# Kernel tuning notes

Measured on AMD Instinct MI355X. Metric: run time of the kernel, lower is better.

## Reference

```python
import jax, jax.numpy as jnp
import numpy as np

# Tree: 64 leaves (16 feat -> 16 out), 8 mids (16 feat + 8*16 child = 144 -> 32 out),
# root (16 feat + 8*32 child = 272 -> 64 out), head -> 10 tasks. Eval-mode BatchNorm.
B = 16384
EPS = 1e-5


def setup_inputs() -> dict:
    key = jax.random.key(0)
    ks = jax.random.split(key, 24)
    rn = lambda k, s: jax.random.normal(k, s, dtype=jnp.float32)
    ru = lambda k, s: jax.random.uniform(k, s, dtype=jnp.float32)
    return {
        "x": rn(ks[0], (B, 1168)),
        # leaf layers (64 nodes, 16 -> 16)
        "Wl": rn(ks[1], (64, 16, 16)) * 0.1, "bl": rn(ks[2], (64, 16)) * 0.1,
        "gl": ru(ks[3], (64, 16)) + 0.5, "betal": rn(ks[4], (64, 16)) * 0.1,
        "ml": rn(ks[5], (64, 16)) * 0.1, "vl": ru(ks[6], (64, 16)) + 0.5,
        # mid layers (8 nodes, 144 -> 32)
        "Wm": rn(ks[7], (8, 144, 32)) * 0.1, "bm": rn(ks[8], (8, 32)) * 0.1,
        "gm": ru(ks[9], (8, 32)) + 0.5, "betam": rn(ks[10], (8, 32)) * 0.1,
        "mm": rn(ks[11], (8, 32)) * 0.1, "vm": ru(ks[12], (8, 32)) + 0.5,
        # root layer (272 -> 64)
        "Wr": rn(ks[13], (272, 64)) * 0.1, "br": rn(ks[14], (64,)) * 0.1,
        "gr": ru(ks[15], (64,)) + 0.5, "betar": rn(ks[16], (64,)) * 0.1,
        "mr": rn(ks[17], (64,)) * 0.1, "vr": ru(ks[18], (64,)) + 0.5,
        # root prediction head (64 -> 10 tasks)
        "Wh": rn(ks[19], (64, 10)) * 0.1, "bh": rn(ks[20], (10,)) * 0.1,
    }


def _bn(h, g, b, m, v):
    return (h - m) * jax.lax.rsqrt(v + EPS) * g + b


def reference(x, Wl, bl, gl, betal, ml, vl, Wm, bm, gm, betam, mm, vm,
              Wr, br, gr, betar, mr, vr, Wh, bh):
    n = x.shape[0]
    # leaves: gather own features (contiguous layout), Linear+BN+Tanh, batched over 64 nodes
    xl = x[:, :1024].reshape(n, 64, 16)
    hl = jnp.tanh(_bn(jnp.einsum('bli,lio->blo', xl, Wl) + bl, gl, betal, ml, vl))
    # mids: concat own features with 8 leaf-child outputs -> [n, 8, 144]
    xm = x[:, 1024:1152].reshape(n, 8, 16)
    mid_in = jnp.concatenate([xm, hl.reshape(n, 8, 128)], axis=-1)
    hm = jnp.tanh(_bn(jnp.einsum('bmi,mio->bmo', mid_in, Wm) + bm, gm, betam, mm, vm))
    # root: concat own features with 8 mid outputs -> [n, 272]
    root_in = jnp.concatenate([x[:, 1152:1168], hm.reshape(n, 256)], axis=-1)
    hr = jnp.tanh(_bn(root_in @ Wr + br, gr, betar, mr, vr))
    # root prediction head (eval-mode forward returns only root prediction)
    return hr @ Wh + bh
```

## Files before the change

### kernel.cpp

```cpp
#include <hip/hip_runtime.h>

typedef __attribute__((ext_vector_type(8))) short bf16x8;
typedef __attribute__((ext_vector_type(4))) float f32x4;

#define EPS 1e-5f
#define K2L 2.8853900817779268f

#define N_FRAG_BLOCKS 182
#define WSB_LEAF 0
#define WSB_MID  64
#define WSB_ROOT 144
#define WSB_HEAD 180
#define ST_SL 0
#define ST_TL 1024
#define ST_SM 2048
#define ST_TM 2304
#define ST_SR 2560
#define ST_TR 2624
#define WS_ST_BYTE_OFF (N_FRAG_BLOCKS * 1024)

__device__ __forceinline__ unsigned short f2bf(float f) {
    unsigned u = __float_as_uint(f);
    unsigned r = u + 0x7fffu + ((u >> 16) & 1u);
    return (unsigned short)(r >> 16);
}

__device__ __forceinline__ unsigned pack2bf(float a, float b) {
    return (unsigned)f2bf(a) | ((unsigned)f2bf(b) << 16);
}

__device__ __forceinline__ bf16x8 pack8(float4 a, float4 b) {
    union { unsigned u[4]; bf16x8 v; } r;
    r.u[0] = pack2bf(a.x, a.y); r.u[1] = pack2bf(a.z, a.w);
    r.u[2] = pack2bf(b.x, b.y); r.u[3] = pack2bf(b.z, b.w);
    return r.v;
}

__device__ __forceinline__ float bn_act(float acc, float Sp, float Tp) {
    float e = exp2f(fmaf(acc, Sp, Tp));
    float r = __builtin_amdgcn_rcpf(e + 1.0f);
    return fmaf(-2.0f, r, 1.0f);
}

__device__ __forceinline__ void gl_lds16(const float* g, float* l) {
    __builtin_amdgcn_global_load_lds(
        (const __attribute__((address_space(1))) unsigned int*)g,
        (__attribute__((address_space(3))) unsigned int*)l, 16, 0, 0);
}

#define FENCE() asm volatile("" ::: "memory")
#define BARRIER() do { FENCE(); __builtin_amdgcn_s_barrier(); FENCE(); } while (0)

__global__ void ontology_prep(
    const float* __restrict__ Wl, const float* __restrict__ Wm,
    const float* __restrict__ Wr, const float* __restrict__ Wh,
    const float* __restrict__ bl, const float* __restrict__ gl,
    const float* __restrict__ betal, const float* __restrict__ ml,
    const float* __restrict__ vl,
    const float* __restrict__ bm, const float* __restrict__ gm,
    const float* __restrict__ betam, const float* __restrict__ mm,
    const float* __restrict__ vm,
    const float* __restrict__ br, const float* __restrict__ gr,
    const float* __restrict__ betar, const float* __restrict__ mr,
    const float* __restrict__ vr,
    unsigned short* __restrict__ wsFrag, float* __restrict__ wsST)
{
    const int b = blockIdx.x;
    const int t = threadIdx.x;
    if (b < N_FRAG_BLOCKS) {
        const int row = t & 15, g = t >> 4;
        unsigned short vals[8];
        #pragma unroll
        for (int i = 0; i < 8; ++i) {
            const int k = g * 8 + i;
            float v = 0.f;
            if (b < 64) {
                const int l = b;
                if ((l & 1) == 0) { if (k < 16)  v = Wl[l * 256 + k * 16 + row]; }
                else              { if (k >= 16) v = Wl[l * 256 + (k - 16) * 16 + row]; }
            } else if (b < 144) {
                const int idx = b - 64, m = idx / 10, rem = idx % 10;
                const int tt = rem / 5, s = rem % 5;
                const int krow = s * 32 + k;
                if (krow < 144) v = Wm[m * 4608 + krow * 32 + tt * 16 + row];
            } else if (b < 180) {
                const int idx = b - 144, tt = idx / 9, s = idx % 9;
                if (s == 0) { if (k < 16) v = Wr[k * 64 + tt * 16 + row]; }
                else { const int krow = 16 + (s - 1) * 32 + k;
                       v = Wr[krow * 64 + tt * 16 + row]; }
            } else {
                const int s = b - 180, krow = s * 32 + k;
                if (row < 10) v = Wh[krow * 10 + row];
            }
            vals[i] = f2bf(v);
        }
        #pragma unroll
        for (int i = 0; i < 8; ++i) wsFrag[b * 512 + t * 8 + i] = vals[i];
    } else if (b == N_FRAG_BLOCKS) {
        for (int i = 0; i < 16; ++i) {
            const int id = t + 64 * i;
            const float S = gl[id] * rsqrtf(vl[id] + EPS);
            wsST[ST_SL + id] = S * K2L;
            wsST[ST_TL + id] = ((bl[id] - ml[id]) * S + betal[id]) * K2L;
        }
    } else if (b == N_FRAG_BLOCKS + 1) {
        for (int i = 0; i < 4; ++i) {
            const int id = t + 64 * i;
            const float S = gm[id] * rsqrtf(vm[id] + EPS);
            wsST[ST_SM + id] = S * K2L;
            wsST[ST_TM + id] = ((bm[id] - mm[id]) * S + betam[id]) * K2L;
        }
    } else {
        const int id = t;
        const float S = gr[id] * rsqrtf(vr[id] + EPS);
        wsST[ST_SR + id] = S * K2L;
        wsST[ST_TR + id] = ((br[id] - mr[id]) * S + betar[id]) * K2L;
    }
}

__global__ __launch_bounds__(256, 4) void ontology_mfma(
    const float* __restrict__ x,
    const unsigned short* __restrict__ wsFrag,
    const float* __restrict__ wsST,
    const float* __restrict__ bh,
    float* __restrict__ out)
{
    __shared__ __align__(16) float xbuf[2][2048];
    __shared__ __align__(16) float xtail[2304];
    __shared__ __align__(16) unsigned short mid_in[16][168];
    __shared__ __align__(16) unsigned short hm[2][16][40];
    unsigned short (*hr)[72] = (unsigned short (*)[72])&xbuf[0][0];

    const int tid  = threadIdx.x;
    const int w    = tid >> 6;
    const int lane = tid & 63;
    const int c    = lane & 15;
    const int g    = lane >> 4;
    const int rowbase = blockIdx.x * 16;
    const float* xbase = x + (size_t)rowbase * 1168;

    const float* Sl = wsST + ST_SL; const float* Tl = wsST + ST_TL;
    const float* Sm = wsST + ST_SM; const float* Tm = wsST + ST_TM;
    const float* Sr = wsST + ST_SR; const float* Tr = wsST + ST_TR;

    int offk[2];
    #pragma unroll
    for (int i = 0; i < 2; ++i) {
        const int k = w * 2 + i;
        const int row = 2 * k + (lane >> 5);
        const int gc = (lane & 31) ^ (row & 7);
        offk[i] = row * 1168 + gc * 4;
    }

    auto stage = [&](int mm) {
        const float* bm_ = xbase + mm * 128;
        float* db = &xbuf[mm & 1][(w * 2) * 256];
        gl_lds16(bm_ + offk[0], db);
        gl_lds16(bm_ + offk[1], db + 256);
    };

    if (w == 1) {
        uint2 z; z.x = 0u; z.y = 0u;
        *(uint2*)&mid_in[c][144 + 4 * g] = z;
    }

    #pragma unroll
    for (int i = 0; i < 2; ++i) {
        const int kk = w + 4 * i;
        const int gi = kk * 64 + lane;
        const int row = gi / 36, col = gi - row * 36;
        gl_lds16(xbase + row * 1168 + 1024 + col * 4, &xtail[kk * 256]);
    }
    if (w == 0) {
        const int gi = 8 * 64 + lane;
        const int row = gi / 36, col = gi - row * 36;
        gl_lds16(xbase + row * 1168 + 1024 + col * 4, &xtail[8 * 256]);
    }
    stage(0);
    stage(1);
    asm volatile("s_waitcnt vmcnt(2) lgkmcnt(0)" ::: "memory");
    BARRIER();

    f32x4 accR;
    {
        const float* rp = &xtail[(c * 36 + 32 + 2 * (g & 1)) * 4];
        float4 xa = *(const float4*)rp;
        float4 xb = *(const float4*)(rp + 4);
        bf16x8 bfrag = pack8(xa, xb);
        bf16x8 a = *(const bf16x8*)(wsFrag + (WSB_ROOT + w * 9) * 512 + lane * 8);
        f32x4 zz = {0.f, 0.f, 0.f, 0.f};
        accR = __builtin_amdgcn_mfma_f32_16x16x32_bf16(a, bfrag, zz, 0, 0, 0);
    }

    #pragma unroll 1
    for (int m = 0; m < 8; ++m) {
        if (m > 0) {
            bf16x8 bfrag = *(const bf16x8*)&hm[(m - 1) & 1][c][g * 8];
            bf16x8 a = *(const bf16x8*)(wsFrag + (WSB_ROOT + w * 9 + m) * 512 + lane * 8);
            accR = __builtin_amdgcn_mfma_f32_16x16x32_bf16(a, bfrag, accR, 0, 0, 0);
        }
        {
            const float* xb_ = &xbuf[m & 1][0];
            const int G0 = w * 8 + g * 2;
            float4 xa = *(const float4*)(xb_ + (c * 32 + (G0 ^ (c & 7))) * 4);
            float4 x2 = *(const float4*)(xb_ + (c * 32 + ((G0 + 1) ^ (c & 7))) * 4);
            bf16x8 bfrag = pack8(xa, x2);
            #pragma unroll
            for (int e = 0; e < 2; ++e) {
                const int leaf = m * 8 + 2 * w + e;
                bf16x8 afrag = *(const bf16x8*)(wsFrag + (WSB_LEAF + leaf) * 512 + lane * 8);
                f32x4 zz = {0.f, 0.f, 0.f, 0.f};
                f32x4 acc = __builtin_amdgcn_mfma_f32_16x16x32_bf16(afrag, bfrag, zz, 0, 0, 0);
                const int po = leaf * 16 + 4 * g;
                float4 S = *(const float4*)(Sl + po);
                float4 T = *(const float4*)(Tl + po);
                float h0 = bn_act(acc[0], S.x, T.x);
                float h1 = bn_act(acc[1], S.y, T.y);
                float h2 = bn_act(acc[2], S.z, T.z);
                float h3 = bn_act(acc[3], S.w, T.w);
                uint2 pk; pk.x = pack2bf(h0, h1); pk.y = pack2bf(h2, h3);
                *(uint2*)&mid_in[c][16 + (2 * w + e) * 16 + 4 * g] = pk;
            }
        }
        if (w == 0) {
            const float* xmp = &xtail[(c * 36 + m * 4 + g) * 4];
            float4 xm4 = *(const float4*)xmp;
            uint2 pm; pm.x = pack2bf(xm4.x, xm4.y); pm.y = pack2bf(xm4.z, xm4.w);
            *(uint2*)&mid_in[c][4 * g] = pm;
        }
        asm volatile("s_waitcnt lgkmcnt(0)" ::: "memory");
        BARRIER();

        if (m + 2 < 8) stage(m + 2);

        if (w >= 2) {
            const int tt = w - 2;
            f32x4 acc = {0.f, 0.f, 0.f, 0.f};
            const unsigned short* fb =
                wsFrag + (WSB_MID + m * 10 + tt * 5) * 512 + lane * 8;
            #pragma unroll
            for (int s = 0; s < 5; ++s) {
                bf16x8 bfrag = *(const bf16x8*)&mid_in[c][s * 32 + g * 8];
                bf16x8 a0 = *(const bf16x8*)(fb + s * 512);
                acc = __builtin_amdgcn_mfma_f32_16x16x32_bf16(a0, bfrag, acc, 0, 0, 0);
            }
            const int po = m * 32 + tt * 16 + 4 * g;
            float4 S = *(const float4*)(Sm + po);
            float4 T = *(const float4*)(Tm + po);
            float h0 = bn_act(acc[0], S.x, T.x);
            float h1 = bn_act(acc[1], S.y, T.y);
            float h2 = bn_act(acc[2], S.z, T.z);
            float h3 = bn_act(acc[3], S.w, T.w);
            uint2 pk; pk.x = pack2bf(h0, h1); pk.y = pack2bf(h2, h3);
            *(uint2*)&hm[m & 1][c][tt * 16 + 4 * g] = pk;
        }
        if (m < 6) { asm volatile("s_waitcnt vmcnt(2)" ::: "memory"); }
        else       { asm volatile("s_waitcnt vmcnt(0)" ::: "memory"); }
        asm volatile("s_waitcnt lgkmcnt(0)" ::: "memory");
        BARRIER();
    }

    {
        bf16x8 bfrag = *(const bf16x8*)&hm[1][c][g * 8];
        bf16x8 a = *(const bf16x8*)(wsFrag + (WSB_ROOT + w * 9 + 8) * 512 + lane * 8);
        accR = __builtin_amdgcn_mfma_f32_16x16x32_bf16(a, bfrag, accR, 0, 0, 0);
        const int po = w * 16 + 4 * g;
        float4 S = *(const float4*)(Sr + po);
        float4 T = *(const float4*)(Tr + po);
        float h0 = bn_act(accR[0], S.x, T.x);
        float h1 = bn_act(accR[1], S.y, T.y);
        float h2 = bn_act(accR[2], S.z, T.z);
        float h3 = bn_act(accR[3], S.w, T.w);
        uint2 pk; pk.x = pack2bf(h0, h1); pk.y = pack2bf(h2, h3);
        *(uint2*)&hr[c][po] = pk;
    }
    asm volatile("s_waitcnt lgkmcnt(0)" ::: "memory");
    BARRIER();

    if (w == 0) {
        f32x4 acc = {0.f, 0.f, 0.f, 0.f};
        #pragma unroll
        for (int s = 0; s < 2; ++s) {
            bf16x8 bfrag = *(const bf16x8*)&hr[c][s * 32 + g * 8];
            bf16x8 a0 = *(const bf16x8*)(wsFrag + (WSB_HEAD + s) * 512 + lane * 8);
            acc = __builtin_amdgcn_mfma_f32_16x16x32_bf16(a0, bfrag, acc, 0, 0, 0);
        }
        float* op = out + (size_t)(rowbase + c) * 10 + 4 * g;
        if (g < 2) {
            float2 o1 = {acc[0] + bh[4 * g],     acc[1] + bh[4 * g + 1]};
            float2 o2 = {acc[2] + bh[4 * g + 2], acc[3] + bh[4 * g + 3]};
            *(float2*)op = o1;
            *(float2*)(op + 2) = o2;
        } else if (g == 2) {
            float2 o1 = {acc[0] + bh[8], acc[1] + bh[9]};
            *(float2*)op = o1;
        }
    }
}

extern "C" void kernel_launch(void* const* d_in, const int* in_sizes, int n_in,
                              void* d_out, int out_size, void* d_ws, size_t ws_size,
                              hipStream_t stream) {
    const float* x     = (const float*)d_in[0];
    const float* Wl    = (const float*)d_in[1];
    const float* bl    = (const float*)d_in[2];
    const float* gl    = (const float*)d_in[3];
    const float* betal = (const float*)d_in[4];
    const float* ml    = (const float*)d_in[5];
    const float* vl    = (const float*)d_in[6];
    const float* Wm    = (const float*)d_in[7];
    const float* bm    = (const float*)d_in[8];
    const float* gm    = (const float*)d_in[9];
    const float* betam = (const float*)d_in[10];
    const float* mm    = (const float*)d_in[11];
    const float* vm    = (const float*)d_in[12];
    const float* Wr    = (const float*)d_in[13];
    const float* br    = (const float*)d_in[14];
    const float* gr    = (const float*)d_in[15];
    const float* betar = (const float*)d_in[16];
    const float* mr    = (const float*)d_in[17];
    const float* vr    = (const float*)d_in[18];
    const float* Wh    = (const float*)d_in[19];
    const float* bh    = (const float*)d_in[20];
    float* out = (float*)d_out;

    unsigned short* wsFrag = (unsigned short*)d_ws;
    float* wsST = (float*)((char*)d_ws + WS_ST_BYTE_OFF);

    ontology_prep<<<N_FRAG_BLOCKS + 3, 64, 0, stream>>>(
        Wl, Wm, Wr, Wh, bl, gl, betal, ml, vl, bm, gm, betam, mm, vm,
        br, gr, betar, mr, vr, wsFrag, wsST);

    const int n = in_sizes[0] / 1168;
    ontology_mfma<<<n / 16, 256, 0, stream>>>(x, wsFrag, wsST, bh, out);
}
```

Baseline: 37.68 us.

## Give each wave whole mid subtrees and read x directly from global memory

```diff
diff --git a/kernel.cpp b/kernel.cpp
--- a/kernel.cpp
+++ b/kernel.cpp
@@ -41,15 +41,6 @@
     float r = __builtin_amdgcn_rcpf(e + 1.0f);
     return fmaf(-2.0f, r, 1.0f);
 }
-
-__device__ __forceinline__ void gl_lds16(const float* g, float* l) {
-    __builtin_amdgcn_global_load_lds(
-        (const __attribute__((address_space(1))) unsigned int*)g,
-        (__attribute__((address_space(3))) unsigned int*)l, 16, 0, 0);
-}
-
-#define FENCE() asm volatile("" ::: "memory")
-#define BARRIER() do { FENCE(); __builtin_amdgcn_s_barrier(); FENCE(); } while (0)
 
 __global__ void ontology_prep(
     const float* __restrict__ Wl, const float* __restrict__ Wm,
@@ -125,11 +116,10 @@
     const float* __restrict__ bh,
     float* __restrict__ out)
 {
-    __shared__ __align__(16) float xbuf[2][2048];
-    __shared__ __align__(16) float xtail[2304];
-    __shared__ __align__(16) unsigned short mid_in[16][168];
-    __shared__ __align__(16) unsigned short hm[2][16][40];
-    unsigned short (*hr)[72] = (unsigned short (*)[72])&xbuf[0][0];
+    __shared__ __align__(16) unsigned short mid_in[4][16][168];
+    __shared__ __align__(16) unsigned short hm[4][16][40];
+    __shared__ __align__(16) float slab[4][16][34];
+    unsigned short (*hr)[72] = (unsigned short (*)[72])&mid_in[0][0][0];
 
     const int tid  = threadIdx.x;
     const int w    = tid >> 6;
@@ -137,80 +127,53 @@
     const int c    = lane & 15;
     const int g    = lane >> 4;
     const int rowbase = blockIdx.x * 16;
-    const float* xbase = x + (size_t)rowbase * 1168;
+    const float* xrow = x + (size_t)(rowbase + c) * 1168;
 
     const float* Sl = wsST + ST_SL; const float* Tl = wsST + ST_TL;
     const float* Sm = wsST + ST_SM; const float* Tm = wsST + ST_TM;
     const float* Sr = wsST + ST_SR; const float* Tr = wsST + ST_TR;
 
-    int offk[2];
+    { uint2 z; z.x = 0u; z.y = 0u; *(uint2*)&mid_in[w][c][144 + 4 * g] = z; }
+
+    f32x4 accR[4];
     #pragma unroll
-    for (int i = 0; i < 2; ++i) {
-        const int k = w * 2 + i;
-        const int row = 2 * k + (lane >> 5);
-        const int gc = (lane & 31) ^ (row & 7);
-        offk[i] = row * 1168 + gc * 4;
-    }
-
-    auto stage = [&](int mm) {
-        const float* bm_ = xbase + mm * 128;
-        float* db = &xbuf[mm & 1][(w * 2) * 256];
-        gl_lds16(bm_ + offk[0], db);
-        gl_lds16(bm_ + offk[1], db + 256);
-    };
-
-    if (w == 1) {
-        uint2 z; z.x = 0u; z.y = 0u;
-        *(uint2*)&mid_in[c][144 + 4 * g] = z;
+    for (int t = 0; t < 4; ++t) { f32x4 z0 = {0.f,0.f,0.f,0.f}; accR[t] = z0; }
+
+    if (w == 3) {
+        const float* rp = xrow + 1152 + (g & 1) * 8;
+        bf16x8 bfrag = pack8(*(const float4*)rp, *(const float4*)(rp + 4));
+        #pragma unroll
+        for (int t = 0; t < 4; ++t) {
+            bf16x8 a = *(const bf16x8*)(wsFrag + (WSB_ROOT + t * 9) * 512 + lane * 8);
+            accR[t] = __builtin_amdgcn_mfma_f32_16x16x32_bf16(a, bfrag, accR[t], 0, 0, 0);
+        }
     }
 
     #pragma unroll
-    for (int i = 0; i < 2; ++i) {
-        const int kk = w + 4 * i;
-        const int gi = kk * 64 + lane;
-        const int row = gi / 36, col = gi - row * 36;
-        gl_lds16(xbase + row * 1168 + 1024 + col * 4, &xtail[kk * 256]);
-    }
-    if (w == 0) {
-        const int gi = 8 * 64 + lane;
-        const int row = gi / 36, col = gi - row * 36;
-        gl_lds16(xbase + row * 1168 + 1024 + col * 4, &xtail[8 * 256]);
-    }
-    stage(0);
-    stage(1);
-    asm volatile("s_waitcnt vmcnt(2) lgkmcnt(0)" ::: "memory");
-    BARRIER();
-
-    f32x4 accR;
-    {
-        const float* rp = &xtail[(c * 36 + 32 + 2 * (g & 1)) * 4];
-        float4 xa = *(const float4*)rp;
-        float4 xb = *(const float4*)(rp + 4);
-        bf16x8 bfrag = pack8(xa, xb);
-        bf16x8 a = *(const bf16x8*)(wsFrag + (WSB_ROOT + w * 9) * 512 + lane * 8);
-        f32x4 zz = {0.f, 0.f, 0.f, 0.f};
-        accR = __builtin_amdgcn_mfma_f32_16x16x32_bf16(a, bfrag, zz, 0, 0, 0);
-    }
-
-    #pragma unroll 1
-    for (int m = 0; m < 8; ++m) {
-        if (m > 0) {
-            bf16x8 bfrag = *(const bf16x8*)&hm[(m - 1) & 1][c][g * 8];
-            bf16x8 a = *(const bf16x8*)(wsFrag + (WSB_ROOT + w * 9 + m) * 512 + lane * 8);
-            accR = __builtin_amdgcn_mfma_f32_16x16x32_bf16(a, bfrag, accR, 0, 0, 0);
-        }
-        {
-            const float* xb_ = &xbuf[m & 1][0];
-            const int G0 = w * 8 + g * 2;
-            float4 xa = *(const float4*)(xb_ + (c * 32 + (G0 ^ (c & 7))) * 4);
-            float4 x2 = *(const float4*)(xb_ + (c * 32 + ((G0 + 1) ^ (c & 7))) * 4);
-            bf16x8 bfrag = pack8(xa, x2);
+    for (int it = 0; it < 2; ++it) {
+        const int M = w + 4 * it;
+        float4 xm4 = *(const float4*)(xrow + 1024 + M * 16 + 4 * g);
+        float4 xp[4][2];
+        #pragma unroll
+        for (int p = 0; p < 4; ++p) {
+            const float* a = xrow + (M * 4 + p) * 32 + g * 8;
+            xp[p][0] = *(const float4*)a;
+            xp[p][1] = *(const float4*)(a + 4);
+        }
+        bf16x8 lfr[8];
+        #pragma unroll
+        for (int l = 0; l < 8; ++l)
+            lfr[l] = *(const bf16x8*)(wsFrag + (WSB_LEAF + M * 8 + l) * 512 + lane * 8);
+        { uint2 pm; pm.x = pack2bf(xm4.x, xm4.y); pm.y = pack2bf(xm4.z, xm4.w);
+          *(uint2*)&mid_in[w][c][4 * g] = pm; }
+        #pragma unroll
+        for (int p = 0; p < 4; ++p) {
+            bf16x8 bfrag = pack8(xp[p][0], xp[p][1]);
             #pragma unroll
             for (int e = 0; e < 2; ++e) {
-                const int leaf = m * 8 + 2 * w + e;
-                bf16x8 afrag = *(const bf16x8*)(wsFrag + (WSB_LEAF + leaf) * 512 + lane * 8);
-                f32x4 zz = {0.f, 0.f, 0.f, 0.f};
-                f32x4 acc = __builtin_amdgcn_mfma_f32_16x16x32_bf16(afrag, bfrag, zz, 0, 0, 0);
+                const int l = 2 * p + e, leaf = M * 8 + l;
+                f32x4 zz = {0.f,0.f,0.f,0.f};
+                f32x4 acc = __builtin_amdgcn_mfma_f32_16x16x32_bf16(lfr[l], bfrag, zz, 0, 0, 0);
                 const int po = leaf * 16 + 4 * g;
                 float4 S = *(const float4*)(Sl + po);
                 float4 T = *(const float4*)(Tl + po);
@@ -219,32 +182,20 @@
                 float h2 = bn_act(acc[2], S.z, T.z);
                 float h3 = bn_act(acc[3], S.w, T.w);
                 uint2 pk; pk.x = pack2bf(h0, h1); pk.y = pack2bf(h2, h3);
-                *(uint2*)&mid_in[c][16 + (2 * w + e) * 16 + 4 * g] = pk;
+                *(uint2*)&mid_in[w][c][16 + l * 16 + 4 * g] = pk;
             }
         }
-        if (w == 0) {
-            const float* xmp = &xtail[(c * 36 + m * 4 + g) * 4];
-            float4 xm4 = *(const float4*)xmp;
-            uint2 pm; pm.x = pack2bf(xm4.x, xm4.y); pm.y = pack2bf(xm4.z, xm4.w);
-            *(uint2*)&mid_in[c][4 * g] = pm;
-        }
-        asm volatile("s_waitcnt lgkmcnt(0)" ::: "memory");
-        BARRIER();
-
-        if (m + 2 < 8) stage(m + 2);
-
-        if (w >= 2) {
-            const int tt = w - 2;
-            f32x4 acc = {0.f, 0.f, 0.f, 0.f};
-            const unsigned short* fb =
-                wsFrag + (WSB_MID + m * 10 + tt * 5) * 512 + lane * 8;
+        #pragma unroll
+        for (int tt = 0; tt < 2; ++tt) {
+            f32x4 acc = {0.f,0.f,0.f,0.f};
+            const unsigned short* fb = wsFrag + (WSB_MID + M * 10 + tt * 5) * 512 + lane * 8;
             #pragma unroll
             for (int s = 0; s < 5; ++s) {
-                bf16x8 bfrag = *(const bf16x8*)&mid_in[c][s * 32 + g * 8];
+                bf16x8 bfrag = *(const bf16x8*)&mid_in[w][c][s * 32 + g * 8];
                 bf16x8 a0 = *(const bf16x8*)(fb + s * 512);
                 acc = __builtin_amdgcn_mfma_f32_16x16x32_bf16(a0, bfrag, acc, 0, 0, 0);
             }
-            const int po = m * 32 + tt * 16 + 4 * g;
+            const int po = M * 32 + tt * 16 + 4 * g;
             float4 S = *(const float4*)(Sm + po);
             float4 T = *(const float4*)(Tm + po);
             float h0 = bn_act(acc[0], S.x, T.x);
@@ -252,33 +203,76 @@
             float h2 = bn_act(acc[2], S.z, T.z);
             float h3 = bn_act(acc[3], S.w, T.w);
             uint2 pk; pk.x = pack2bf(h0, h1); pk.y = pack2bf(h2, h3);
-            *(uint2*)&hm[m & 1][c][tt * 16 + 4 * g] = pk;
-        }
-        if (m < 6) { asm volatile("s_waitcnt vmcnt(2)" ::: "memory"); }
-        else       { asm volatile("s_waitcnt vmcnt(0)" ::: "memory"); }
-        asm volatile("s_waitcnt lgkmcnt(0)" ::: "memory");
-        BARRIER();
-    }
-
-    {
-        bf16x8 bfrag = *(const bf16x8*)&hm[1][c][g * 8];
-        bf16x8 a = *(const bf16x8*)(wsFrag + (WSB_ROOT + w * 9 + 8) * 512 + lane * 8);
-        accR = __builtin_amdgcn_mfma_f32_16x16x32_bf16(a, bfrag, accR, 0, 0, 0);
+            *(uint2*)&hm[w][c][tt * 16 + 4 * g] = pk;
+        }
+        {
+            bf16x8 bfrag = *(const bf16x8*)&hm[w][c][g * 8];
+            #pragma unroll
+            for (int t = 0; t < 4; ++t) {
+                bf16x8 a = *(const bf16x8*)(wsFrag + (WSB_ROOT + t * 9 + M + 1) * 512 + lane * 8);
+                accR[t] = __builtin_amdgcn_mfma_f32_16x16x32_bf16(a, bfrag, accR[t], 0, 0, 0);
+            }
+        }
+    }
+
+    #pragma unroll
+    for (int t = 0; t < 2; ++t) {
+        float2 lo; lo.x = accR[t][0]; lo.y = accR[t][1];
+        float2 hi; hi.x = accR[t][2]; hi.y = accR[t][3];
+        *(float2*)&slab[w][c][t * 16 + 4 * g]     = lo;
+        *(float2*)&slab[w][c][t * 16 + 4 * g + 2] = hi;
+    }
+    asm volatile("s_waitcnt lgkmcnt(0)" ::: "memory");
+    __builtin_amdgcn_s_barrier();
+    if (w < 2) {
+        float4 sum = {0.f,0.f,0.f,0.f};
+        #pragma unroll
+        for (int v = 0; v < 4; ++v) {
+            float2 lo = *(const float2*)&slab[v][c][w * 16 + 4 * g];
+            float2 hi = *(const float2*)&slab[v][c][w * 16 + 4 * g + 2];
+            sum.x += lo.x; sum.y += lo.y; sum.z += hi.x; sum.w += hi.y;
+        }
         const int po = w * 16 + 4 * g;
         float4 S = *(const float4*)(Sr + po);
         float4 T = *(const float4*)(Tr + po);
-        float h0 = bn_act(accR[0], S.x, T.x);
-        float h1 = bn_act(accR[1], S.y, T.y);
-        float h2 = bn_act(accR[2], S.z, T.z);
-        float h3 = bn_act(accR[3], S.w, T.w);
-        uint2 pk; pk.x = pack2bf(h0, h1); pk.y = pack2bf(h2, h3);
+        uint2 pk;
+        pk.x = pack2bf(bn_act(sum.x, S.x, T.x), bn_act(sum.y, S.y, T.y));
+        pk.y = pack2bf(bn_act(sum.z, S.z, T.z), bn_act(sum.w, S.w, T.w));
         *(uint2*)&hr[c][po] = pk;
     }
     asm volatile("s_waitcnt lgkmcnt(0)" ::: "memory");
-    BARRIER();
+    __builtin_amdgcn_s_barrier();
+
+    #pragma unroll
+    for (int t = 2; t < 4; ++t) {
+        float2 lo; lo.x = accR[t][0]; lo.y = accR[t][1];
+        float2 hi; hi.x = accR[t][2]; hi.y = accR[t][3];
+        *(float2*)&slab[w][c][(t - 2) * 16 + 4 * g]     = lo;
+        *(float2*)&slab[w][c][(t - 2) * 16 + 4 * g + 2] = hi;
+    }
+    asm volatile("s_waitcnt lgkmcnt(0)" ::: "memory");
+    __builtin_amdgcn_s_barrier();
+    if (w >= 2) {
+        float4 sum = {0.f,0.f,0.f,0.f};
+        #pragma unroll
+        for (int v = 0; v < 4; ++v) {
+            float2 lo = *(const float2*)&slab[v][c][(w - 2) * 16 + 4 * g];
+            float2 hi = *(const float2*)&slab[v][c][(w - 2) * 16 + 4 * g + 2];
+            sum.x += lo.x; sum.y += lo.y; sum.z += hi.x; sum.w += hi.y;
+        }
+        const int po = w * 16 + 4 * g;
+        float4 S = *(const float4*)(Sr + po);
+        float4 T = *(const float4*)(Tr + po);
+        uint2 pk;
+        pk.x = pack2bf(bn_act(sum.x, S.x, T.x), bn_act(sum.y, S.y, T.y));
+        pk.y = pack2bf(bn_act(sum.z, S.z, T.z), bn_act(sum.w, S.w, T.w));
+        *(uint2*)&hr[c][po] = pk;
+    }
+    asm volatile("s_waitcnt lgkmcnt(0)" ::: "memory");
+    __builtin_amdgcn_s_barrier();
 
     if (w == 0) {
-        f32x4 acc = {0.f, 0.f, 0.f, 0.f};
+        f32x4 acc = {0.f,0.f,0.f,0.f};
         #pragma unroll
         for (int s = 0; s < 2; ++s) {
             bf16x8 bfrag = *(const bf16x8*)&hr[c][s * 32 + g * 8];
```

New measurement: 31.61 us. 16.1% less time.
